# Kernel optimization log

Hardware: AMD Instinct MI355X
Metric: run time of the kernel (lower is better)

The kernel has to match this reference:

```python
import jax, jax.numpy as jnp
import numpy as np

N = 100000      # nodes
E = 1600000     # edges
DIN, DH, DOUT = 128, 256, 40


def setup_inputs() -> dict:
    key = jax.random.key(0)
    ks = jax.random.split(key, 24)

    def w(i, fan_in, fan_out):
        s = 1.0 / np.sqrt(fan_in)
        return jax.random.uniform(ks[i], (fan_in, fan_out), jnp.float32, -s, s)

    def b(i, fan_in, fan_out):
        s = 1.0 / np.sqrt(fan_in)
        return jax.random.uniform(ks[i], (fan_out,), jnp.float32, -s, s)

    return {
        "x": jax.random.normal(ks[0], (N, DIN), jnp.float32),
        "edge_index": jax.random.randint(ks[1], (2, E), 0, N, dtype=jnp.int64),
        # updates_continues: Linear(DIN,DH), Linear(DH,DH), Linear(DH,DOUT)
        "Wc0": w(2, DIN, DH),  "bc0": b(3, DIN, DH),
        "Wc1": w(4, DH, DH),   "bc1": b(5, DH, DH),
        "Wc2": w(6, DH, DOUT), "bc2": b(7, DH, DOUT),
        # updates_exit: Linear(DIN,DOUT) x2, Linear(DH,DOUT) x2
        "We0": w(8, DIN, DOUT),  "be0": b(9, DIN, DOUT),
        "We1": w(10, DIN, DOUT), "be1": b(11, DIN, DOUT),
        "We2": w(12, DH, DOUT),  "be2": b(13, DH, DOUT),
        "We3": w(14, DH, DOUT),  "be3": b(15, DH, DOUT),
    }


def _gcn_agg(h, src, dst):
    """Symmetric-normalized GCN aggregation with self-loops: D^-1/2 (A+I) D^-1/2 h."""
    ones = jnp.ones(src.shape[0], h.dtype)
    deg = jax.ops.segment_sum(ones, dst, num_segments=N) + 1.0  # self-loop
    dinv = jax.lax.rsqrt(deg)
    coef = dinv[src] * dinv[dst]                    # [E]
    msgs = h[src] * coef[:, None]                   # [E, d] gather
    out = jax.ops.segment_sum(msgs, dst, num_segments=N)  # scatter-add
    return out + h * (dinv * dinv)[:, None]         # self-loop term


def reference(x, edge_index, Wc0, bc0, Wc1, bc1, Wc2, bc2,
              We0, be0, We1, be1, We2, be2, We3, be3):
    src, dst = edge_index[0], edge_index[1]
    Wc = [(Wc0, bc0), (Wc1, bc1), (Wc2, bc2)]
    We = [(We0, be0), (We1, be1), (We2, be2), (We3, be3)]

    h = x
    outs = [jax.nn.log_softmax(h @ We[0][0] + We[0][1], axis=1)]
    for i in range(3):
        h = _gcn_agg(h, src, dst)
        outs.append(jax.nn.log_softmax(h @ We[i + 1][0] + We[i + 1][1], axis=1))
        h = h @ Wc[i][0] + Wc[i][1]
        if i < 2:
            h = jax.nn.relu(h)  # dropout is identity in eval mode
    return jnp.stack(outs, axis=1)  # [N, num_layers+1, DOUT]
```

## Files before the change

kernel.cpp:

```cpp
#include <hip/hip_runtime.h>

#define NNODES 100000
#define NEDGES 1600000
#define NBKT 782

typedef __attribute__((ext_vector_type(8))) short bf16x8;
typedef __attribute__((ext_vector_type(4))) float f32x4;

__device__ __forceinline__ float bf2f(unsigned v) {
  union { unsigned u; float f; } x; x.u = v << 16; return x.f;
}
__device__ __forceinline__ unsigned short f2bf(float f) {
  union { float f; unsigned u; } x; x.f = f;
  unsigned r = x.u + 0x7fffu + ((x.u >> 16) & 1u);
  return (unsigned short)(r >> 16);
}

__global__ void k_probe(const unsigned* __restrict__ xw, const int* __restrict__ ei,
                        int* __restrict__ flags) {
  __shared__ int cF, cI;
  if (threadIdx.x == 0) { cF = 0; cI = 0; }
  __syncthreads();
  int t = threadIdx.x;
  int hf = 0;
  for (int i = t; i < 2048; i += 256) {
    unsigned lo = xw[i] & 0xffffu;
    unsigned e = (lo >> 7) & 0xffu;
    if (e >= 0xC0u) hf++;
  }
  atomicAdd(&cF, hf);
  int hi = 0;
  if (ei[2 * t + 1] != 0) hi++;
  atomicAdd(&cI, hi);
  __syncthreads();
  if (threadIdx.x == 0) {
    flags[0] = (cF > 32) ? 1 : 0;
    flags[1] = (cI < 16) ? 1 : 0;
  }
}

__device__ __forceinline__ int edge_at(const int* __restrict__ ei, int j, int i64) {
  return i64 ? ei[2 * j] : ei[j];
}

struct CvtParams {
  const void* src[13];
  unsigned short* dst[13];
  int n[13];
};

__global__ void k_cvt(CvtParams p, const int* __restrict__ flags) {
  int a = blockIdx.y;
  int n = p.n[a];
  int f32 = flags[0];
  const float* sf = (const float*)p.src[a];
  const unsigned short* sb = (const unsigned short*)p.src[a];
  unsigned short* d = p.dst[a];
  for (int i = blockIdx.x * blockDim.x + threadIdx.x; i < n; i += gridDim.x * blockDim.x) {
    d[i] = f32 ? f2bf(sf[i]) : sb[i];
  }
}

__global__ void k_transpose(const unsigned short* __restrict__ W,
                            unsigned short* __restrict__ WT, int K) {
  int idx = blockIdx.x * 256 + threadIdx.x;
  if (idx < K * 256) {
    int k = idx >> 8, c = idx & 255;
    WT[c * K + k] = W[idx];
  }
}

template <int K>
__global__ void k_transpose40(const unsigned short* __restrict__ W,
                              unsigned short* __restrict__ WT) {
  int idx = blockIdx.x * 256 + threadIdx.x;
  if (idx < 48 * K) {
    int c = idx / K, k = idx % K;
    WT[idx] = (c < 40) ? W[k * 40 + c] : (unsigned short)0;
  }
}

__global__ void k_zero(int* __restrict__ p, int n) {
  int v = blockIdx.x * blockDim.x + threadIdx.x;
  if (v < n) p[v] = 0;
}


__global__ __launch_bounds__(256) void k_bcnt(const int* __restrict__ ei,
                                              int* __restrict__ bcnt,
                                              const int* __restrict__ flags) {
  __shared__ int h[NBKT];
  int t = threadIdx.x;
  for (int i = t; i < NBKT; i += 256) h[i] = 0;
  __syncthreads();
  int i64 = flags[1];
  int e0 = blockIdx.x * 4096;
#pragma unroll
  for (int k = 0; k < 16; ++k) {
    int e = e0 + t + k * 256;
    if (e < NEDGES) {
      int d = edge_at(ei, NEDGES + e, i64);
      if ((unsigned)d < NNODES) atomicAdd(&h[d >> 7], 1);
    }
  }
  __syncthreads();
  for (int i = t; i < NBKT; i += 256)
    if (h[i]) atomicAdd(&bcnt[i], h[i]);
}

__global__ void k_bscan2(const int* __restrict__ bcnt, int* __restrict__ bbase,
                         int* __restrict__ gcur) {
  int l = threadIdx.x;
  int v[13];
  int s = 0;
#pragma unroll
  for (int k = 0; k < 13; ++k) {
    int j = l * 13 + k;
    v[k] = (j < NBKT) ? bcnt[j] : 0;
    s += v[k];
  }
  int x = s;
#pragma unroll
  for (int o = 1; o < 64; o <<= 1) {
    int y = __shfl_up(x, o, 64);
    if (l >= o) x += y;
  }
  int excl = x - s;
#pragma unroll
  for (int k = 0; k < 13; ++k) {
    int j = l * 13 + k;
    if (j < NBKT) { bbase[j] = excl; gcur[j] = excl; }
    excl += v[k];
  }
  if (l == 63) bbase[NBKT] = x;
}

__global__ __launch_bounds__(256) void k_bstage(const int* __restrict__ ei,
                                                int* __restrict__ gcur,
                                                int* __restrict__ stage,
                                                const int* __restrict__ flags) {
  __shared__ int h[NBKT];
  __shared__ int base[NBKT];
  int t = threadIdx.x;
  for (int i = t; i < NBKT; i += 256) h[i] = 0;
  __syncthreads();
  int i64 = flags[1];
  int e0 = blockIdx.x * 4096;
  int bkt[16], lp[16], rec[16];
#pragma unroll
  for (int k = 0; k < 16; ++k) {
    bkt[k] = -1;
    int e = e0 + t + k * 256;
    if (e < NEDGES) {
      int d = edge_at(ei, NEDGES + e, i64);
      if ((unsigned)d < NNODES) {
        int s = edge_at(ei, e, i64);
        if ((unsigned)s >= NNODES) s = NNODES - 1;
        bkt[k] = d >> 7;
        rec[k] = ((d & 127) << 17) | s;
        lp[k] = atomicAdd(&h[bkt[k]], 1);
      }
    }
  }
  __syncthreads();
  for (int i = t; i < NBKT; i += 256)
    base[i] = h[i] ? atomicAdd(&gcur[i], h[i]) : 0;
  __syncthreads();
#pragma unroll
  for (int k = 0; k < 16; ++k)
    if (bkt[k] >= 0) stage[base[bkt[k]] + lp[k]] = rec[k];
}

__global__ __launch_bounds__(256) void k_bplace(const int* __restrict__ stage,
                                                const int* __restrict__ bbase,
                                                int* __restrict__ offs,
                                                float* __restrict__ dinv,
                                                int* __restrict__ csr_src) {
  __shared__ int h[128];
  __shared__ int cur[128];
  int b = blockIdx.x;
  int t = threadIdx.x;
  int n0 = b * 128;
  int NN = NNODES - n0; if (NN > 128) NN = 128;
  int s0 = bbase[b], s1 = bbase[b + 1];
  int cnt = s1 - s0;
  if (t < 128) h[t] = 0;
  __syncthreads();
  for (int i = t; i < cnt; i += 256) {
    int rec = stage[s0 + i];
    atomicAdd(&h[rec >> 17], 1);
  }
  __syncthreads();
  if (t < 64) {
    int a = h[2 * t], c = h[2 * t + 1];
    int s = a + c;
    int x = s;
#pragma unroll
    for (int o = 1; o < 64; o <<= 1) {
      int y = __shfl_up(x, o, 64);
      if (t >= o) x += y;
    }
    int excl = s0 + x - s;
    cur[2 * t] = excl;
    cur[2 * t + 1] = excl + a;
    if (2 * t < NN) {
      offs[n0 + 2 * t] = excl;
      dinv[n0 + 2 * t] = rsqrtf((float)a + 1.0f);
    }
    if (2 * t + 1 < NN) {
      offs[n0 + 2 * t + 1] = excl + a;
      dinv[n0 + 2 * t + 1] = rsqrtf((float)c + 1.0f);
    }
  }
  if (b == NBKT - 1 && t == 0) offs[NNODES] = s1;
  __syncthreads();
  for (int i = t; i < cnt; i += 256) {
    int rec = stage[s0 + i];
    int pos = atomicAdd(&cur[rec >> 17], 1);
    csr_src[pos] = rec & 0x1FFFF;
  }
}

__device__ __forceinline__ void acc8(float (&acc)[8], uint4 u, float w) {
  acc[0] += w * bf2f(u.x & 0xffffu);
  acc[1] += w * bf2f(u.x >> 16);
  acc[2] += w * bf2f(u.y & 0xffffu);
  acc[3] += w * bf2f(u.y >> 16);
  acc[4] += w * bf2f(u.z & 0xffffu);
  acc[5] += w * bf2f(u.z >> 16);
  acc[6] += w * bf2f(u.w & 0xffffu);
  acc[7] += w * bf2f(u.w >> 16);
}

template <int D, bool GDINV>
__global__ __launch_bounds__(256) void k_agg(
    const unsigned short* __restrict__ hin, unsigned short* __restrict__ hout,
    const int* __restrict__ offs, const int* __restrict__ csr_src,
    const float* __restrict__ dinv) {
  constexpr int LPR = D / 8;
  constexpr int R = 64 / LPR;
  constexpr int NB = 8 / R;
  const int lane = threadIdx.x & 63;
  const int g = lane / LPR;
  const int l = lane % LPR;
  const int v = (blockIdx.x * 256 + threadIdx.x) >> 6;
  if (v >= NNODES) return;

  float dv = dinv[v];
  const size_t vbase = (size_t)v * D + l * 8;
  uint4 su = *(const uint4*)(hin + vbase);
  float acc[8];
#pragma unroll
  for (int k = 0; k < 8; ++k) acc[k] = 0.f;
  acc8(acc, su, (g == 0) ? (GDINV ? dv : 1.f) : 0.f);

  int b0 = offs[v];
  int n = offs[v + 1] - b0;
  for (int i = 0; i < n; i += 8) {
    int s[NB];
    float wg[NB];
#pragma unroll
    for (int j = 0; j < NB; ++j) {
      int ei = i + j * R + g;
      int ec = (ei < n) ? ei : (n - 1);
      s[j] = csr_src[b0 + ec];
      wg[j] = (ei < n) ? (GDINV ? dinv[s[j]] : 1.f) : 0.f;
    }
    uint4 gu[NB];
#pragma unroll
    for (int j = 0; j < NB; ++j)
      gu[j] = *(const uint4*)(hin + (size_t)s[j] * D + l * 8);
#pragma unroll
    for (int j = 0; j < NB; ++j) acc8(acc, gu[j], wg[j]);
  }
#pragma unroll
  for (int k = 0; k < 8; ++k) {
#pragma unroll
    for (int o = LPR; o < 64; o <<= 1) acc[k] += __shfl_xor(acc[k], o, 64);
  }
  if (g == 0) {
    uint4 ov;
    ov.x = (unsigned)f2bf(dv * acc[0]) | ((unsigned)f2bf(dv * acc[1]) << 16);
    ov.y = (unsigned)f2bf(dv * acc[2]) | ((unsigned)f2bf(dv * acc[3]) << 16);
    ov.z = (unsigned)f2bf(dv * acc[4]) | ((unsigned)f2bf(dv * acc[5]) << 16);
    ov.w = (unsigned)f2bf(dv * acc[6]) | ((unsigned)f2bf(dv * acc[7]) << 16);
    *(uint4*)(hout + vbase) = ov;
  }
}

__global__ __launch_bounds__(256) void k_agg40(
    const unsigned short* __restrict__ P, const int* __restrict__ offs,
    const int* __restrict__ csr_src, const float* __restrict__ dinv,
    const unsigned short* __restrict__ bias, float* __restrict__ outp) {
  const int lane = threadIdx.x & 63;
  const int g = lane >> 5, l = lane & 31;
  const bool act = l < 20;
  const int v = (blockIdx.x * 256 + threadIdx.x) >> 6;
  if (v >= NNODES) return;

  float dv = dinv[v];
  float a0 = 0.f, a1 = 0.f;
  if (act && g == 0) {
    unsigned su = *(const unsigned*)(P + (size_t)v * 40 + l * 2);
    a0 = bf2f(su & 0xffffu);
    a1 = bf2f(su >> 16);
  }
  int b0 = offs[v];
  int n = offs[v + 1] - b0;
  for (int i = 0; i < n; i += 8) {
    int s[4];
    float wg[4];
#pragma unroll
    for (int j = 0; j < 4; ++j) {
      int ei = i + j * 2 + g;
      int ec = (ei < n) ? ei : (n - 1);
      s[j] = csr_src[b0 + ec];
      wg[j] = (ei < n) ? 1.f : 0.f;
    }
    unsigned gu[4];
#pragma unroll
    for (int j = 0; j < 4; ++j)
      gu[j] = act ? *(const unsigned*)(P + (size_t)s[j] * 40 + l * 2) : 0u;
#pragma unroll
    for (int j = 0; j < 4; ++j) {
      a0 += wg[j] * bf2f(gu[j] & 0xffffu);
      a1 += wg[j] * bf2f(gu[j] >> 16);
    }
  }
  a0 += __shfl_xor(a0, 32, 64);
  a1 += __shfl_xor(a1, 32, 64);
  if (act) {
    a0 = dv * a0 + bf2f((unsigned)bias[l * 2]);
    a1 = dv * a1 + bf2f((unsigned)bias[l * 2 + 1]);
  }
  float m = act ? fmaxf(a0, a1) : -1e30f;
#pragma unroll
  for (int o = 16; o > 0; o >>= 1) m = fmaxf(m, __shfl_xor(m, o, 32));
  float ss = act ? (expf(a0 - m) + expf(a1 - m)) : 0.f;
#pragma unroll
  for (int o = 16; o > 0; o >>= 1) ss += __shfl_xor(ss, o, 32);
  float ls = logf(ss) + m;
  if (act && g == 0) {
    float2 o2;
    o2.x = a0 - ls;
    o2.y = a1 - ls;
    *(float2*)(outp + (size_t)v * 160 + l * 2) = o2;
  }
}

template <int K, bool SCALE>
__global__ __launch_bounds__(256) void k_mlp_mfma(
    const unsigned short* __restrict__ A, const unsigned short* __restrict__ WT,
    const unsigned short* __restrict__ bias, unsigned short* __restrict__ out,
    const float* __restrict__ dinv) {
  __shared__ short As[128 * 40];
  __shared__ short Bs[128 * 40];
  const int t = threadIdx.x;
  const int lane = t & 63, wv = t >> 6;
  const int m0 = blockIdx.x * 128;
  const int c0 = blockIdx.y * 128;
  const int mw = (wv >> 1) * 64, nw = (wv & 1) * 64;
  const int lr = lane & 15, lq = lane >> 4;

  f32x4 acc[4][4];
#pragma unroll
  for (int i = 0; i < 4; ++i)
#pragma unroll
    for (int j = 0; j < 4; ++j) acc[i][j] = (f32x4)0.f;

  for (int kc = 0; kc < K; kc += 32) {
    __syncthreads();
#pragma unroll
    for (int it = 0; it < 2; ++it) {
      int idx = t + it * 256;
      int row = idx >> 2, seg = idx & 3;
      uint4 u = make_uint4(0, 0, 0, 0);
      int gr = m0 + row;
      if (gr < NNODES) u = *(const uint4*)(A + (size_t)gr * K + kc + seg * 8);
      *(uint4*)&As[row * 40 + seg * 8] = u;
      uint4 v = *(const uint4*)(WT + (size_t)(c0 + row) * K + kc + seg * 8);
      *(uint4*)&Bs[row * 40 + seg * 8] = v;
    }
    __syncthreads();
    bf16x8 af[4], bfr[4];
#pragma unroll
    for (int i = 0; i < 4; ++i)
      af[i] = *(const bf16x8*)&As[(mw + 16 * i + lr) * 40 + lq * 8];
#pragma unroll
    for (int j = 0; j < 4; ++j)
      bfr[j] = *(const bf16x8*)&Bs[(nw + 16 * j + lr) * 40 + lq * 8];
#pragma unroll
    for (int i = 0; i < 4; ++i)
#pragma unroll
      for (int j = 0; j < 4; ++j)
        acc[i][j] = __builtin_amdgcn_mfma_f32_16x16x32_bf16(af[i], bfr[j], acc[i][j], 0, 0, 0);
  }

  float bv[4];
#pragma unroll
  for (int j = 0; j < 4; ++j) bv[j] = bf2f((unsigned)bias[c0 + nw + 16 * j + lr]);
#pragma unroll
  for (int i = 0; i < 4; ++i) {
    int rbase = m0 + mw + 16 * i + lq * 4;
#pragma unroll
    for (int r = 0; r < 4; ++r) {
      int row = rbase + r;
      if (row < NNODES) {
        float s = SCALE ? dinv[row] : 1.f;
#pragma unroll
        for (int j = 0; j < 4; ++j) {
          int col = c0 + nw + 16 * j + lr;
          float v = fmaxf(acc[i][j][r] + bv[j], 0.f) * s;
          out[(size_t)row * 256 + col] = f2bf(v);
        }
      }
    }
  }
}

template <int K, bool SOFTMAX>
__global__ __launch_bounds__(256) void k_exit_mfma(
    const unsigned short* __restrict__ A, const unsigned short* __restrict__ WT,
    const unsigned short* __restrict__ bias, float* __restrict__ outp,
    unsigned short* __restrict__ Pout, const float* __restrict__ dinv) {
  constexpr int KP = K + 8;
  __shared__ short As[128 * 40];
  __shared__ short Bs[48 * KP];
  const int t = threadIdx.x;
  const int lane = t & 63, wv = t >> 6;
  const int m0 = blockIdx.x * 128;
  const int mw = wv * 32;
  const int lr = lane & 15, lq = lane >> 4;

  for (int idx = t; idx < 48 * (K / 8); idx += 256) {
    int row = idx / (K / 8), seg = idx % (K / 8);
    uint4 w = *(const uint4*)(WT + (size_t)row * K + seg * 8);
    *(uint4*)&Bs[row * KP + seg * 8] = w;
  }

  f32x4 acc[2][3];
#pragma unroll
  for (int i = 0; i < 2; ++i)
#pragma unroll
    for (int j = 0; j < 3; ++j) acc[i][j] = (f32x4)0.f;

  for (int kc = 0; kc < K; kc += 32) {
    __syncthreads();
#pragma unroll
    for (int it = 0; it < 2; ++it) {
      int idx = t + it * 256;
      int row = idx >> 2, seg = idx & 3;
      uint4 u = make_uint4(0, 0, 0, 0);
      int gr = m0 + row;
      if (gr < NNODES) u = *(const uint4*)(A + (size_t)gr * K + kc + seg * 8);
      *(uint4*)&As[row * 40 + seg * 8] = u;
    }
    __syncthreads();
    bf16x8 af[2], bfr[3];
#pragma unroll
    for (int i = 0; i < 2; ++i)
      af[i] = *(const bf16x8*)&As[(mw + 16 * i + lr) * 40 + lq * 8];
#pragma unroll
    for (int j = 0; j < 3; ++j)
      bfr[j] = *(const bf16x8*)&Bs[(16 * j + lr) * KP + kc + lq * 8];
#pragma unroll
    for (int i = 0; i < 2; ++i)
#pragma unroll
      for (int j = 0; j < 3; ++j)
        acc[i][j] = __builtin_amdgcn_mfma_f32_16x16x32_bf16(af[i], bfr[j], acc[i][j], 0, 0, 0);
  }

  if (SOFTMAX) {
    float bv0 = bf2f((unsigned)bias[lr]);
    float bv1 = bf2f((unsigned)bias[16 + lr]);
    float bv2 = (lr < 8) ? bf2f((unsigned)bias[32 + lr]) : 0.f;
#pragma unroll
    for (int i = 0; i < 2; ++i) {
#pragma unroll
      for (int r = 0; r < 4; ++r) {
        int row = m0 + mw + 16 * i + lq * 4 + r;
        float v0 = acc[i][0][r] + bv0;
        float v1 = acc[i][1][r] + bv1;
        float v2 = (lr < 8) ? (acc[i][2][r] + bv2) : -1e30f;
        float m = fmaxf(fmaxf(v0, v1), v2);
#pragma unroll
        for (int o = 8; o > 0; o >>= 1) m = fmaxf(m, __shfl_xor(m, o, 16));
        float ss = expf(v0 - m) + expf(v1 - m) + ((lr < 8) ? expf(v2 - m) : 0.f);
#pragma unroll
        for (int o = 8; o > 0; o >>= 1) ss += __shfl_xor(ss, o, 16);
        float ls = logf(ss) + m;
        if (row < NNODES) {
          outp[(size_t)row * 160 + lr] = v0 - ls;
          outp[(size_t)row * 160 + 16 + lr] = v1 - ls;
          if (lr < 8) outp[(size_t)row * 160 + 32 + lr] = v2 - ls;
        }
      }
    }
  } else {
#pragma unroll
    for (int i = 0; i < 2; ++i) {
#pragma unroll
      for (int r = 0; r < 4; ++r) {
        int row = m0 + mw + 16 * i + lq * 4 + r;
        if (row < NNODES) {
          float s = dinv[row];
          Pout[(size_t)row * 40 + lr] = f2bf(acc[i][0][r] * s);
          Pout[(size_t)row * 40 + 16 + lr] = f2bf(acc[i][1][r] * s);
          if (lr < 8) Pout[(size_t)row * 40 + 32 + lr] = f2bf(acc[i][2][r] * s);
        }
      }
    }
  }
}

extern "C" void kernel_launch(void* const* d_in, const int* in_sizes, int n_in,
                              void* d_out, int out_size, void* d_ws, size_t ws_size,
                              hipStream_t stream) {
  const void* x_raw   = d_in[0];
  const int* ei       = (const int*)d_in[1];
  float* out          = (float*)d_out;

  char* ws = (char*)d_ws;
  int*   flags    = (int*)(ws + 0);
  int*   bcnt     = (int*)(ws + 4096);
  int*   gcur     = (int*)(ws + 8192);
  int*   bbase    = (int*)(ws + 12288);
  float* dinv     = (float*)(ws + 524288);
  int*   offs     = (int*)(ws + 1048576);
  int*   csr_src  = (int*)(ws + 2097152);
  int*   stage    = (int*)(ws + 8650752);
  unsigned short* xb = (unsigned short*)(ws + 16777216);
  unsigned short* wb = (unsigned short*)(ws + 45088768);
  unsigned short* hA = (unsigned short*)(ws + 48234496);
  unsigned short* hB = (unsigned short*)(ws + 100663296);
  unsigned short* P  = xb;

  unsigned short* Wc0 = wb + 0;
  unsigned short* bc0 = wb + 32768;
  unsigned short* Wc1 = wb + 33024;
  unsigned short* bc1 = wb + 98560;
  unsigned short* We0 = wb + 98816;
  unsigned short* be0 = wb + 103936;
  unsigned short* We1 = wb + 103976;
  unsigned short* be1 = wb + 109096;
  unsigned short* We2 = wb + 109136;
  unsigned short* be2 = wb + 119376;
  unsigned short* We3 = wb + 119416;
  unsigned short* be3 = wb + 129656;
  unsigned short* WTc0  = wb + 131072;
  unsigned short* WTc1  = wb + 163840;
  unsigned short* WT40e0 = wb + 229376;
  unsigned short* WT40e1 = wb + 235520;
  unsigned short* WT40e2 = wb + 241664;
  unsigned short* WT40e3 = wb + 253952;

  dim3 B(256);
  k_probe<<<dim3(1), B, 0, stream>>>((const unsigned*)x_raw, ei, flags);
  k_zero<<<dim3(4), B, 0, stream>>>(bcnt, NBKT);

  CvtParams p;
  const int srcIdx[13] = {0, 2, 3, 4, 5, 8, 9, 10, 11, 12, 13, 14, 15};
  unsigned short* dsts[13] = {xb, Wc0, bc0, Wc1, bc1, We0, be0, We1, be1, We2, be2, We3, be3};
  const int ns[13] = {NNODES * 128, 128 * 256, 256, 256 * 256, 256,
                      128 * 40, 40, 128 * 40, 40, 256 * 40, 40, 256 * 40, 40};
  for (int i = 0; i < 13; ++i) { p.src[i] = d_in[srcIdx[i]]; p.dst[i] = dsts[i]; p.n[i] = ns[i]; }
  k_cvt<<<dim3(1024, 13), B, 0, stream>>>(p, flags);
  k_transpose<<<dim3(128), B, 0, stream>>>(Wc0, WTc0, 128);
  k_transpose<<<dim3(256), B, 0, stream>>>(Wc1, WTc1, 256);
  k_transpose40<128><<<dim3(24), B, 0, stream>>>(We0, WT40e0);
  k_transpose40<128><<<dim3(24), B, 0, stream>>>(We1, WT40e1);
  k_transpose40<256><<<dim3(48), B, 0, stream>>>(We2, WT40e2);
  k_transpose40<256><<<dim3(48), B, 0, stream>>>(We3, WT40e3);

  k_bcnt<<<dim3(391), B, 0, stream>>>(ei, bcnt, flags);
  k_bscan2<<<dim3(1), dim3(64), 0, stream>>>(bcnt, bbase, gcur);
  k_bstage<<<dim3(391), B, 0, stream>>>(ei, gcur, stage, flags);
  k_bplace<<<dim3(NBKT), B, 0, stream>>>(stage, bbase, offs, dinv, csr_src);

  k_exit_mfma<128, true><<<dim3(782), B, 0, stream>>>(xb, WT40e0, be0, out + 0 * 40, nullptr, dinv);
  k_agg<128, true><<<dim3(25000), B, 0, stream>>>(xb, hA, offs, csr_src, dinv);
  k_exit_mfma<128, true><<<dim3(782), B, 0, stream>>>(hA, WT40e1, be1, out + 1 * 40, nullptr, dinv);
  k_mlp_mfma<128, true><<<dim3(782, 2), B, 0, stream>>>(hA, WTc0, bc0, hB, dinv);
  k_agg<256, false><<<dim3(25000), B, 0, stream>>>(hB, hA, offs, csr_src, dinv);
  k_exit_mfma<256, true><<<dim3(782), B, 0, stream>>>(hA, WT40e2, be2, out + 2 * 40, nullptr, dinv);
  k_mlp_mfma<256, false><<<dim3(782, 2), B, 0, stream>>>(hA, WTc1, bc1, hB, nullptr);
  k_exit_mfma<256, false><<<dim3(782), B, 0, stream>>>(hB, WT40e3, nullptr, nullptr, P, dinv);
  k_agg40<<<dim3(25000), B, 0, stream>>>(P, offs, csr_src, dinv, be3, out + 3 * 40);
}
```

Before: 630.4 us.

## Prescale x by dinv, prefetch CSR indices, merge prep kernels, packed bf16 accumulation

Several changes land together. The CSR build now runs before conversion so k_cvt can also write a dinv-prescaled bf16 copy of x, which drops the per-edge dinv gather in the first aggregation. Both aggregation kernels software-pipeline the next batch of source indices while the current gathers are in flight, and accumulate with packed float2 ops. The first layer now gathers 16 edges per batch instead of 8. The bcnt zeroing moves into the probe kernel and the six transposes merge into one launch, cutting launch overhead at the cost of an extra 100000x128 write in k_cvt.

```diff
diff --git a/kernel.cpp b/kernel.cpp
--- a/kernel.cpp
+++ b/kernel.cpp
@@ -6,6 +6,7 @@
 
 typedef __attribute__((ext_vector_type(8))) short bf16x8;
 typedef __attribute__((ext_vector_type(4))) float f32x4;
+typedef __attribute__((ext_vector_type(2))) float f32x2;
 
 __device__ __forceinline__ float bf2f(unsigned v) {
   union { unsigned u; float f; } x; x.u = v << 16; return x.f;
@@ -15,9 +16,14 @@
   unsigned r = x.u + 0x7fffu + ((x.u >> 16) & 1u);
   return (unsigned short)(r >> 16);
 }
+__device__ __forceinline__ f32x2 unpk(unsigned u) {
+  union { unsigned q; float f; } lo, hi;
+  lo.q = u << 16; hi.q = u & 0xffff0000u;
+  f32x2 r; r.x = lo.f; r.y = hi.f; return r;
+}
 
 __global__ void k_probe(const unsigned* __restrict__ xw, const int* __restrict__ ei,
-                        int* __restrict__ flags) {
+                        int* __restrict__ flags, int* __restrict__ bcnt) {
   __shared__ int cF, cI;
   if (threadIdx.x == 0) { cF = 0; cI = 0; }
   __syncthreads();
@@ -32,6 +38,7 @@
   int hi = 0;
   if (ei[2 * t + 1] != 0) hi++;
   atomicAdd(&cI, hi);
+  for (int i = t; i < NBKT; i += 256) bcnt[i] = 0;
   __syncthreads();
   if (threadIdx.x == 0) {
     flags[0] = (cF > 32) ? 1 : 0;
@@ -49,7 +56,8 @@
   int n[13];
 };
 
-__global__ void k_cvt(CvtParams p, const int* __restrict__ flags) {
+__global__ void k_cvt(CvtParams p, const int* __restrict__ flags,
+                      const float* __restrict__ dinv, unsigned short* __restrict__ xs) {
   int a = blockIdx.y;
   int n = p.n[a];
   int f32 = flags[0];
@@ -57,32 +65,32 @@
   const unsigned short* sb = (const unsigned short*)p.src[a];
   unsigned short* d = p.dst[a];
   for (int i = blockIdx.x * blockDim.x + threadIdx.x; i < n; i += gridDim.x * blockDim.x) {
-    d[i] = f32 ? f2bf(sf[i]) : sb[i];
-  }
-}
-
-__global__ void k_transpose(const unsigned short* __restrict__ W,
-                            unsigned short* __restrict__ WT, int K) {
+    if (a == 0) {
+      float v = f32 ? sf[i] : bf2f((unsigned)sb[i]);
+      d[i] = f32 ? f2bf(v) : sb[i];
+      xs[i] = f2bf(v * dinv[i >> 7]);
+    } else {
+      d[i] = f32 ? f2bf(sf[i]) : sb[i];
+    }
+  }
+}
+
+__global__ void k_wprep(const unsigned short* __restrict__ Wc0, unsigned short* __restrict__ WTc0,
+                        const unsigned short* __restrict__ Wc1, unsigned short* __restrict__ WTc1,
+                        const unsigned short* __restrict__ We0, unsigned short* __restrict__ WT40e0,
+                        const unsigned short* __restrict__ We1, unsigned short* __restrict__ WT40e1,
+                        const unsigned short* __restrict__ We2, unsigned short* __restrict__ WT40e2,
+                        const unsigned short* __restrict__ We3, unsigned short* __restrict__ WT40e3) {
+  int job = blockIdx.y;
   int idx = blockIdx.x * 256 + threadIdx.x;
-  if (idx < K * 256) {
-    int k = idx >> 8, c = idx & 255;
-    WT[c * K + k] = W[idx];
-  }
-}
-
-template <int K>
-__global__ void k_transpose40(const unsigned short* __restrict__ W,
-                              unsigned short* __restrict__ WT) {
-  int idx = blockIdx.x * 256 + threadIdx.x;
-  if (idx < 48 * K) {
-    int c = idx / K, k = idx % K;
-    WT[idx] = (c < 40) ? W[k * 40 + c] : (unsigned short)0;
-  }
-}
-
-__global__ void k_zero(int* __restrict__ p, int n) {
-  int v = blockIdx.x * blockDim.x + threadIdx.x;
-  if (v < n) p[v] = 0;
+  switch (job) {
+    case 0: if (idx < 128 * 256) { int k = idx >> 8, c = idx & 255; WTc0[c * 128 + k] = Wc0[idx]; } break;
+    case 1: if (idx < 256 * 256) { int k = idx >> 8, c = idx & 255; WTc1[c * 256 + k] = Wc1[idx]; } break;
+    case 2: if (idx < 48 * 128) { int c = idx / 128, k = idx % 128; WT40e0[idx] = (c < 40) ? We0[k * 40 + c] : (unsigned short)0; } break;
+    case 3: if (idx < 48 * 128) { int c = idx / 128, k = idx % 128; WT40e1[idx] = (c < 40) ? We1[k * 40 + c] : (unsigned short)0; } break;
+    case 4: if (idx < 48 * 256) { int c = idx / 256, k = idx % 256; WT40e2[idx] = (c < 40) ? We2[k * 40 + c] : (unsigned short)0; } break;
+    case 5: if (idx < 48 * 256) { int c = idx / 256, k = idx % 256; WT40e3[idx] = (c < 40) ? We3[k * 40 + c] : (unsigned short)0; } break;
+  }
 }
 
 
@@ -221,25 +229,21 @@
   }
 }
 
-__device__ __forceinline__ void acc8(float (&acc)[8], uint4 u, float w) {
-  acc[0] += w * bf2f(u.x & 0xffffu);
-  acc[1] += w * bf2f(u.x >> 16);
-  acc[2] += w * bf2f(u.y & 0xffffu);
-  acc[3] += w * bf2f(u.y >> 16);
-  acc[4] += w * bf2f(u.z & 0xffffu);
-  acc[5] += w * bf2f(u.z >> 16);
-  acc[6] += w * bf2f(u.w & 0xffffu);
-  acc[7] += w * bf2f(u.w >> 16);
-}
-
-template <int D, bool GDINV>
+__device__ __forceinline__ void accp(f32x2 (&acc)[4], uint4 u, float w) {
+  acc[0] += unpk(u.x) * w;
+  acc[1] += unpk(u.y) * w;
+  acc[2] += unpk(u.z) * w;
+  acc[3] += unpk(u.w) * w;
+}
+
+template <int D, int EPB>
 __global__ __launch_bounds__(256) void k_agg(
     const unsigned short* __restrict__ hin, unsigned short* __restrict__ hout,
     const int* __restrict__ offs, const int* __restrict__ csr_src,
     const float* __restrict__ dinv) {
   constexpr int LPR = D / 8;
   constexpr int R = 64 / LPR;
-  constexpr int NB = 8 / R;
+  constexpr int NB = EPB / R;
   const int lane = threadIdx.x & 63;
   const int g = lane / LPR;
   const int l = lane % LPR;
@@ -249,41 +253,57 @@
   float dv = dinv[v];
   const size_t vbase = (size_t)v * D + l * 8;
   uint4 su = *(const uint4*)(hin + vbase);
-  float acc[8];
-#pragma unroll
-  for (int k = 0; k < 8; ++k) acc[k] = 0.f;
-  acc8(acc, su, (g == 0) ? (GDINV ? dv : 1.f) : 0.f);
+  f32x2 acc[4];
+#pragma unroll
+  for (int k = 0; k < 4; ++k) acc[k] = (f32x2)0.f;
+  accp(acc, su, (g == 0) ? 1.f : 0.f);
 
   int b0 = offs[v];
   int n = offs[v + 1] - b0;
-  for (int i = 0; i < n; i += 8) {
+  if (n > 0) {
     int s[NB];
     float wg[NB];
 #pragma unroll
     for (int j = 0; j < NB; ++j) {
-      int ei = i + j * R + g;
-      int ec = (ei < n) ? ei : (n - 1);
+      int e = j * R + g;
+      int ec = (e < n) ? e : (n - 1);
       s[j] = csr_src[b0 + ec];
-      wg[j] = (ei < n) ? (GDINV ? dinv[s[j]] : 1.f) : 0.f;
-    }
-    uint4 gu[NB];
-#pragma unroll
-    for (int j = 0; j < NB; ++j)
-      gu[j] = *(const uint4*)(hin + (size_t)s[j] * D + l * 8);
-#pragma unroll
-    for (int j = 0; j < NB; ++j) acc8(acc, gu[j], wg[j]);
-  }
+      wg[j] = (e < n) ? 1.f : 0.f;
+    }
+    for (int i = 0; i < n; i += EPB) {
+      uint4 gu[NB];
+#pragma unroll
+      for (int j = 0; j < NB; ++j)
+        gu[j] = *(const uint4*)(hin + (size_t)s[j] * D + l * 8);
+      float wc[NB];
+#pragma unroll
+      for (int j = 0; j < NB; ++j) wc[j] = wg[j];
+      int i2 = i + EPB;
+#pragma unroll
+      for (int j = 0; j < NB; ++j) {
+        int e = i2 + j * R + g;
+        int ec = (e < n) ? e : (n - 1);
+        s[j] = csr_src[b0 + ec];
+        wg[j] = (e < n) ? 1.f : 0.f;
+      }
+#pragma unroll
+      for (int j = 0; j < NB; ++j) accp(acc, gu[j], wc[j]);
+    }
+  }
+  float a8[8];
+#pragma unroll
+  for (int k = 0; k < 4; ++k) { a8[2 * k] = acc[k].x; a8[2 * k + 1] = acc[k].y; }
 #pragma unroll
   for (int k = 0; k < 8; ++k) {
 #pragma unroll
-    for (int o = LPR; o < 64; o <<= 1) acc[k] += __shfl_xor(acc[k], o, 64);
+    for (int o = LPR; o < 64; o <<= 1) a8[k] += __shfl_xor(a8[k], o, 64);
   }
   if (g == 0) {
     uint4 ov;
-    ov.x = (unsigned)f2bf(dv * acc[0]) | ((unsigned)f2bf(dv * acc[1]) << 16);
-    ov.y = (unsigned)f2bf(dv * acc[2]) | ((unsigned)f2bf(dv * acc[3]) << 16);
-    ov.z = (unsigned)f2bf(dv * acc[4]) | ((unsigned)f2bf(dv * acc[5]) << 16);
-    ov.w = (unsigned)f2bf(dv * acc[6]) | ((unsigned)f2bf(dv * acc[7]) << 16);
+    ov.x = (unsigned)f2bf(dv * a8[0]) | ((unsigned)f2bf(dv * a8[1]) << 16);
+    ov.y = (unsigned)f2bf(dv * a8[2]) | ((unsigned)f2bf(dv * a8[3]) << 16);
+    ov.z = (unsigned)f2bf(dv * a8[4]) | ((unsigned)f2bf(dv * a8[5]) << 16);
+    ov.w = (unsigned)f2bf(dv * a8[6]) | ((unsigned)f2bf(dv * a8[7]) << 16);
     *(uint4*)(hout + vbase) = ov;
   }
 }
@@ -299,39 +319,46 @@
   if (v >= NNODES) return;
 
   float dv = dinv[v];
-  float a0 = 0.f, a1 = 0.f;
-  if (act && g == 0) {
-    unsigned su = *(const unsigned*)(P + (size_t)v * 40 + l * 2);
-    a0 = bf2f(su & 0xffffu);
-    a1 = bf2f(su >> 16);
-  }
+  f32x2 a = (f32x2)0.f;
+  if (act && g == 0) a = unpk(*(const unsigned*)(P + (size_t)v * 40 + l * 2));
   int b0 = offs[v];
   int n = offs[v + 1] - b0;
-  for (int i = 0; i < n; i += 8) {
+  if (n > 0) {
     int s[4];
     float wg[4];
 #pragma unroll
     for (int j = 0; j < 4; ++j) {
-      int ei = i + j * 2 + g;
-      int ec = (ei < n) ? ei : (n - 1);
+      int e = j * 2 + g;
+      int ec = (e < n) ? e : (n - 1);
       s[j] = csr_src[b0 + ec];
-      wg[j] = (ei < n) ? 1.f : 0.f;
-    }
-    unsigned gu[4];
-#pragma unroll
-    for (int j = 0; j < 4; ++j)
-      gu[j] = act ? *(const unsigned*)(P + (size_t)s[j] * 40 + l * 2) : 0u;
-#pragma unroll
-    for (int j = 0; j < 4; ++j) {
-      a0 += wg[j] * bf2f(gu[j] & 0xffffu);
-      a1 += wg[j] * bf2f(gu[j] >> 16);
-    }
-  }
-  a0 += __shfl_xor(a0, 32, 64);
-  a1 += __shfl_xor(a1, 32, 64);
+      wg[j] = (e < n) ? 1.f : 0.f;
+    }
+    for (int i = 0; i < n; i += 8) {
+      unsigned gu[4];
+#pragma unroll
+      for (int j = 0; j < 4; ++j)
+        gu[j] = act ? *(const unsigned*)(P + (size_t)s[j] * 40 + l * 2) : 0u;
+      float wc[4];
+#pragma unroll
+      for (int j = 0; j < 4; ++j) wc[j] = wg[j];
+      int i2 = i + 8;
+#pragma unroll
+      for (int j = 0; j < 4; ++j) {
+        int e = i2 + j * 2 + g;
+        int ec = (e < n) ? e : (n - 1);
+        s[j] = csr_src[b0 + ec];
+        wg[j] = (e < n) ? 1.f : 0.f;
+      }
+#pragma unroll
+      for (int j = 0; j < 4; ++j) a += unpk(gu[j]) * wc[j];
+    }
+  }
+  a.x += __shfl_xor(a.x, 32, 64);
+  a.y += __shfl_xor(a.y, 32, 64);
+  float a0 = 0.f, a1 = 0.f;
   if (act) {
-    a0 = dv * a0 + bf2f((unsigned)bias[l * 2]);
-    a1 = dv * a1 + bf2f((unsigned)bias[l * 2 + 1]);
+    a0 = dv * a.x + bf2f((unsigned)bias[l * 2]);
+    a1 = dv * a.y + bf2f((unsigned)bias[l * 2 + 1]);
   }
   float m = act ? fmaxf(a0, a1) : -1e30f;
 #pragma unroll
@@ -533,6 +560,7 @@
   unsigned short* wb = (unsigned short*)(ws + 45088768);
   unsigned short* hA = (unsigned short*)(ws + 48234496);
   unsigned short* hB = (unsigned short*)(ws + 100663296);
+  unsigned short* xs = hB;
   unsigned short* P  = xb;
 
   unsigned short* Wc0 = wb + 0;
@@ -555,8 +583,12 @@
   unsigned short* WT40e3 = wb + 253952;
 
   dim3 B(256);
-  k_probe<<<dim3(1), B, 0, stream>>>((const unsigned*)x_raw, ei, flags);
-  k_zero<<<dim3(4), B, 0, stream>>>(bcnt, NBKT);
+  k_probe<<<dim3(1), B, 0, stream>>>((const unsigned*)x_raw, ei, flags, bcnt);
+
+  k_bcnt<<<dim3(391), B, 0, stream>>>(ei, bcnt, flags);
+  k_bscan2<<<dim3(1), dim3(64), 0, stream>>>(bcnt, bbase, gcur);
+  k_bstage<<<dim3(391), B, 0, stream>>>(ei, gcur, stage, flags);
+  k_bplace<<<dim3(NBKT), B, 0, stream>>>(stage, bbase, offs, dinv, csr_src);
 
   CvtParams p;
   const int srcIdx[13] = {0, 2, 3, 4, 5, 8, 9, 10, 11, 12, 13, 14, 15};
@@ -564,24 +596,15 @@
   const int ns[13] = {NNODES * 128, 128 * 256, 256, 256 * 256, 256,
                       128 * 40, 40, 128 * 40, 40, 256 * 40, 40, 256 * 40, 40};
   for (int i = 0; i < 13; ++i) { p.src[i] = d_in[srcIdx[i]]; p.dst[i] = dsts[i]; p.n[i] = ns[i]; }
-  k_cvt<<<dim3(1024, 13), B, 0, stream>>>(p, flags);
-  k_transpose<<<dim3(128), B, 0, stream>>>(Wc0, WTc0, 128);
-  k_transpose<<<dim3(256), B, 0, stream>>>(Wc1, WTc1, 256);
-  k_transpose40<128><<<dim3(24), B, 0, stream>>>(We0, WT40e0);
-  k_transpose40<128><<<dim3(24), B, 0, stream>>>(We1, WT40e1);
-  k_transpose40<256><<<dim3(48), B, 0, stream>>>(We2, WT40e2);
-  k_transpose40<256><<<dim3(48), B, 0, stream>>>(We3, WT40e3);
-
-  k_bcnt<<<dim3(391), B, 0, stream>>>(ei, bcnt, flags);
-  k_bscan2<<<dim3(1), dim3(64), 0, stream>>>(bcnt, bbase, gcur);
-  k_bstage<<<dim3(391), B, 0, stream>>>(ei, gcur, stage, flags);
-  k_bplace<<<dim3(NBKT), B, 0, stream>>>(stage, bbase, offs, dinv, csr_src);
+  k_cvt<<<dim3(1024, 13), B, 0, stream>>>(p, flags, dinv, xs);
+  k_wprep<<<dim3(256, 6), B, 0, stream>>>(Wc0, WTc0, Wc1, WTc1, We0, WT40e0,
+                                          We1, WT40e1, We2, WT40e2, We3, WT40e3);
 
   k_exit_mfma<128, true><<<dim3(782), B, 0, stream>>>(xb, WT40e0, be0, out + 0 * 40, nullptr, dinv);
-  k_agg<128, true><<<dim3(25000), B, 0, stream>>>(xb, hA, offs, csr_src, dinv);
+  k_agg<128, 16><<<dim3(25000), B, 0, stream>>>(xs, hA, offs, csr_src, dinv);
   k_exit_mfma<128, true><<<dim3(782), B, 0, stream>>>(hA, WT40e1, be1, out + 1 * 40, nullptr, dinv);
   k_mlp_mfma<128, true><<<dim3(782, 2), B, 0, stream>>>(hA, WTc0, bc0, hB, dinv);
-  k_agg<256, false><<<dim3(25000), B, 0, stream>>>(hB, hA, offs, csr_src, dinv);
+  k_agg<256, 8><<<dim3(25000), B, 0, stream>>>(hB, hA, offs, csr_src, dinv);
   k_exit_mfma<256, true><<<dim3(782), B, 0, stream>>>(hA, WT40e2, be2, out + 2 * 40, nullptr, dinv);
   k_mlp_mfma<256, false><<<dim3(782, 2), B, 0, stream>>>(hA, WTc1, bc1, hB, nullptr);
   k_exit_mfma<256, false><<<dim3(782), B, 0, stream>>>(hB, WT40e3, nullptr, nullptr, P, dinv);
```

After: 636.8 us. No clear change (+1.0%).
